# Performance work log

Measured on AMD Instinct MI355X. Metric: run time of the kernel, lower is better.

## Reference

```python
import jax, jax.numpy as jnp
import numpy as np

EMBED_DIM = 1024
NUM_HEADS = 16
HEAD_DIM = EMBED_DIM // NUM_HEADS  # 64
NUM_FEATURES = 32
POLY_DIM = 16
NUM_QUAD = 2
EPS = 1e-06
C = 2.0 + EPS
B = 4096


def setup_inputs() -> dict:
    key = jax.random.key(0)
    kx, k1, k2 = jax.random.split(key, 3)
    x = jax.random.normal(kx, (B, EMBED_DIM), dtype=jnp.float32)
    omega = jax.random.normal(k1, (NUM_QUAD, NUM_HEADS, HEAD_DIM, NUM_FEATURES), dtype=jnp.float32)
    omega = omega / jnp.sqrt(float(HEAD_DIM))
    anchors = jax.random.normal(k2, (POLY_DIM, HEAD_DIM), dtype=jnp.float32)
    anchors = anchors / jnp.linalg.norm(anchors, axis=-1, keepdims=True)
    nodes, weights = np.polynomial.laguerre.laggauss(NUM_QUAD)
    nodes = np.maximum(nodes, 0.01)
    weights = np.maximum(weights, 0.01)
    quad_nodes = jnp.array(nodes, dtype=jnp.float32) / C
    quad_weights = jnp.array(weights, dtype=jnp.float32) / C
    return {"x": x, "omega": omega, "anchors": anchors,
            "quad_nodes": quad_nodes, "quad_weights": quad_weights}


def reference(x, omega, anchors, quad_nodes, quad_weights):
    Bsz = x.shape[0]
    # [B, H, D], safe-normalize over head_dim
    xr = x.reshape(Bsz, NUM_HEADS, HEAD_DIM)
    norm = jnp.linalg.norm(xr, axis=-1, keepdims=True)
    xn = xr / jnp.maximum(norm, 1e-4)
    # polynomial features: [B, H, P]
    poly_proj = jnp.clip(jnp.einsum('bhd,pd->bhp', xn, anchors), -1.0, 1.0)
    poly_feat = poly_proj ** 2 / jnp.sqrt(float(POLY_DIM))
    # positive random features: [R, B, H, M]
    prf_proj = jnp.einsum('bhd,rhdm->rbhm', xn, omega)
    s = jnp.maximum(quad_nodes.reshape(-1, 1, 1, 1), 1e-06)
    exp_arg = jnp.clip(prf_proj * jnp.sqrt(2.0 * s) - s, -20.0, 20.0)
    prf_feat = jnp.exp(exp_arg) / jnp.sqrt(NUM_FEATURES + 1e-06)
    prf_feat = prf_feat * jnp.sqrt(jnp.maximum(quad_weights.reshape(-1, 1, 1, 1), 1e-06))
    # fused outer product over quadrature nodes: [R, B, H, P, M]
    fused = poly_feat[None, :, :, :, None] * prf_feat[:, :, :, None, :]
    # concat over r along last axis == r-major flatten: [B, R*H*P*M]
    return jnp.transpose(fused, (1, 0, 2, 3, 4)).reshape(Bsz, -1)
```

## Files before the change

### kernel.cpp

```cpp
#include <hip/hip_runtime.h>

#define NHEADS 16
#define HDIM   64
#define NFEAT  32
#define PDIM   16
#define NQUAD  2
#define GB     8
#define WAVES_PB 4

typedef float f32x4 __attribute__((ext_vector_type(4)));

__global__ __launch_bounds__(256, 3)
void slay_kernel(const float* __restrict__ x,
                 const float* __restrict__ omega,
                 const float* __restrict__ anchors,
                 const float* __restrict__ qn,
                 const float* __restrict__ qw,
                 float* __restrict__ out)
{
    __shared__ __align__(16) float s_xn [WAVES_PB][64];
    __shared__ __align__(16) float s_prf[WAVES_PB][64];
    __shared__ __align__(16) float s_poly[WAVES_PB][16];

    const int tid  = threadIdx.x;
    const int wv   = tid >> 6;
    const int lane = tid & 63;
    const int h    = blockIdx.x & 15;
    const int b0   = ((blockIdx.x >> 4) * WAVES_PB + wv) * GB;

    const int r = lane >> 5;
    const int m = lane & 31;
    const int p = lane & 15;
    const int g = lane >> 4;

    const float sR     = fmaxf(qn[r], 1e-6f);
    const float sq2s   = sqrtf(2.0f * sR);
    const float scaleR = sqrtf(fmaxf(qw[r], 1e-6f)) / sqrtf(32.0f + 1e-6f);

    float om[64];
    {
        const float* oc = omega + ((size_t)(r * NHEADS + h) * HDIM) * NFEAT + m;
        #pragma unroll
        for (int d = 0; d < 64; ++d) om[d] = oc[(size_t)d * NFEAT];
    }
    float an[16];
    {
        const float* ac = anchors + p * HDIM + g * 16;
        #pragma unroll
        for (int dd = 0; dd < 16; ++dd) an[dd] = ac[dd];
    }

    float xvv[GB];
    {
        const float* xb = x + (size_t)b0 * (NHEADS * HDIM) + h * HDIM + lane;
        #pragma unroll
        for (int bb = 0; bb < GB; ++bb) xvv[bb] = xb[(size_t)bb * (NHEADS * HDIM)];
    }

    #pragma unroll
    for (int bb = 0; bb < GB; ++bb) {
        const int b = b0 + bb;

        float ss = xvv[bb] * xvv[bb];
        #pragma unroll
        for (int off = 32; off > 0; off >>= 1) ss += __shfl_xor(ss, off, 64);
        const float xn = xvv[bb] / fmaxf(sqrtf(ss), 1e-4f);

        __builtin_amdgcn_wave_barrier();
        s_xn[wv][lane] = xn;
        __builtin_amdgcn_wave_barrier();

        float a0 = 0.f, a1 = 0.f, a2 = 0.f, a3 = 0.f;
        #pragma unroll
        for (int d = 0; d < 64; d += 4) {
            const float s0 = __uint_as_float(__builtin_amdgcn_readlane(__float_as_uint(xn), d + 0));
            const float s1 = __uint_as_float(__builtin_amdgcn_readlane(__float_as_uint(xn), d + 1));
            const float s2 = __uint_as_float(__builtin_amdgcn_readlane(__float_as_uint(xn), d + 2));
            const float s3 = __uint_as_float(__builtin_amdgcn_readlane(__float_as_uint(xn), d + 3));
            a0 = fmaf(s0, om[d + 0], a0);
            a1 = fmaf(s1, om[d + 1], a1);
            a2 = fmaf(s2, om[d + 2], a2);
            a3 = fmaf(s3, om[d + 3], a3);
        }
        const float accR = (a0 + a1) + (a2 + a3);

        float p0 = 0.f, p1 = 0.f, p2 = 0.f, p3 = 0.f;
        #pragma unroll
        for (int q4 = 0; q4 < 4; ++q4) {
            const f32x4 xq = *(const f32x4*)&s_xn[wv][g * 16 + q4 * 4];
            p0 = fmaf(xq.x, an[q4 * 4 + 0], p0);
            p1 = fmaf(xq.y, an[q4 * 4 + 1], p1);
            p2 = fmaf(xq.z, an[q4 * 4 + 2], p2);
            p3 = fmaf(xq.w, an[q4 * 4 + 3], p3);
        }
        float accP = (p0 + p1) + (p2 + p3);
        accP += __shfl_xor(accP, 16, 64);
        accP += __shfl_xor(accP, 32, 64);

        const float arg  = fminf(fmaxf(accR * sq2s - sR, -20.f), 20.f);
        const float prf  = expf(arg) * scaleR;
        const float pc   = fminf(fmaxf(accP, -1.f), 1.f);
        const float poly = pc * pc * 0.25f;

        __builtin_amdgcn_wave_barrier();
        s_prf[wv][lane] = prf;
        if (lane < 16) s_poly[wv][lane] = poly;
        __builtin_amdgcn_wave_barrier();

        float* ob = out + (size_t)b * (NQUAD * NHEADS * PDIM * NFEAT)
                        + (size_t)h * (PDIM * NFEAT);
        #pragma unroll
        for (int i4 = 0; i4 < 4; ++i4) {
            const int rr = i4 >> 1;
            const int pp = (i4 * 8 + (lane >> 3)) & 15;
            const float pf = s_poly[wv][pp];
            const f32x4 pr = *(const f32x4*)&s_prf[wv][rr * 32 + (lane & 7) * 4];
            f32x4 v;
            v.x = pf * pr.x; v.y = pf * pr.y; v.z = pf * pr.z; v.w = pf * pr.w;
            *(f32x4*)(ob + (size_t)rr * (NHEADS * PDIM * NFEAT)
                         + (i4 & 1) * 256 + lane * 4) = v;
        }
    }
}

extern "C" void kernel_launch(void* const* d_in, const int* in_sizes, int n_in,
                              void* d_out, int out_size, void* d_ws, size_t ws_size,
                              hipStream_t stream)
{
    const float* x       = (const float*)d_in[0];
    const float* omega   = (const float*)d_in[1];
    const float* anchors = (const float*)d_in[2];
    const float* qn      = (const float*)d_in[3];
    const float* qw      = (const float*)d_in[4];
    float* out = (float*)d_out;

    const int Bsz = in_sizes[0] / (NHEADS * HDIM);
    dim3 grid((Bsz / (WAVES_PB * GB)) * NHEADS);
    slay_kernel<<<grid, 256, 0, stream>>>(x, omega, anchors, qn, qw, out);
}
```

Measured before the change: 62.65 us.

## Split into feature kernel plus coalesced expand kernel via workspace

Computes prf and poly features in a first kernel and stores them in a workspace buffer. A second elementwise kernel then writes the outer-product output with fully linear, coalesced f32x4 stores. The goal is to separate the compute-heavy feature stage from the write-bandwidth-bound expansion so each can run at its own occupancy. The cost is extra workspace traffic and a second launch, and the old fused kernel is kept as a fallback when the workspace is too small.

Measured after the change: 76.15 us. 21.5% more time.

```diff
diff --git a/kernel.cpp b/kernel.cpp
--- a/kernel.cpp
+++ b/kernel.cpp
@@ -11,16 +11,15 @@
 typedef float f32x4 __attribute__((ext_vector_type(4)));
 
 __global__ __launch_bounds__(256, 3)
-void slay_kernel(const float* __restrict__ x,
-                 const float* __restrict__ omega,
-                 const float* __restrict__ anchors,
-                 const float* __restrict__ qn,
-                 const float* __restrict__ qw,
-                 float* __restrict__ out)
-{
-    __shared__ __align__(16) float s_xn [WAVES_PB][64];
-    __shared__ __align__(16) float s_prf[WAVES_PB][64];
-    __shared__ __align__(16) float s_poly[WAVES_PB][16];
+void slay_features(const float* __restrict__ x,
+                   const float* __restrict__ omega,
+                   const float* __restrict__ anchors,
+                   const float* __restrict__ qn,
+                   const float* __restrict__ qw,
+                   float* __restrict__ prf_ws,
+                   float* __restrict__ poly_ws)
+{
+    __shared__ __align__(16) float s_xn[WAVES_PB][64];
 
     const int tid  = threadIdx.x;
     const int wv   = tid >> 6;
@@ -102,6 +101,128 @@
         const float pc   = fminf(fmaxf(accP, -1.f), 1.f);
         const float poly = pc * pc * 0.25f;
 
+        prf_ws[(size_t)b * 1024 + r * 512 + h * 32 + m] = prf;
+        if (lane < 16)
+            poly_ws[(size_t)b * 256 + h * 16 + p] = poly;
+    }
+}
+
+__global__ __launch_bounds__(256)
+void slay_expand(const float* __restrict__ prf_ws,
+                 const float* __restrict__ poly_ws,
+                 float* __restrict__ out)
+{
+    const f32x4* __restrict__ prf4 = (const f32x4*)prf_ws;
+    f32x4* __restrict__ out4 = (f32x4*)out;
+
+    const int j0 = blockIdx.x * 1024 + threadIdx.x;
+    #pragma unroll
+    for (int k = 0; k < 4; ++k) {
+        const int j = j0 + k * 256;
+        const int b  = j >> 12;
+        const int q  = j & 4095;
+        const int rr = q >> 11;
+        const int hh = (q >> 7) & 15;
+        const int pp = (q >> 3) & 15;
+        const int mg = q & 7;
+        const float pf = poly_ws[(b << 8) | (hh << 4) | pp];
+        const f32x4 pr = prf4[(b << 8) | (rr << 7) | (hh << 3) | mg];
+        f32x4 v;
+        v.x = pf * pr.x; v.y = pf * pr.y; v.z = pf * pr.z; v.w = pf * pr.w;
+        out4[j] = v;
+    }
+}
+
+__global__ __launch_bounds__(256, 3)
+void slay_fused(const float* __restrict__ x,
+                const float* __restrict__ omega,
+                const float* __restrict__ anchors,
+                const float* __restrict__ qn,
+                const float* __restrict__ qw,
+                float* __restrict__ out)
+{
+    __shared__ __align__(16) float s_xn [WAVES_PB][64];
+    __shared__ __align__(16) float s_prf[WAVES_PB][64];
+    __shared__ __align__(16) float s_poly[WAVES_PB][16];
+
+    const int tid  = threadIdx.x;
+    const int wv   = tid >> 6;
+    const int lane = tid & 63;
+    const int h    = blockIdx.x & 15;
+    const int b0   = ((blockIdx.x >> 4) * WAVES_PB + wv) * GB;
+
+    const int r = lane >> 5;
+    const int m = lane & 31;
+    const int p = lane & 15;
+    const int g = lane >> 4;
+
+    const float sR     = fmaxf(qn[r], 1e-6f);
+    const float sq2s   = sqrtf(2.0f * sR);
+    const float scaleR = sqrtf(fmaxf(qw[r], 1e-6f)) / sqrtf(32.0f + 1e-6f);
+
+    float om[64];
+    {
+        const float* oc = omega + ((size_t)(r * NHEADS + h) * HDIM) * NFEAT + m;
+        #pragma unroll
+        for (int d = 0; d < 64; ++d) om[d] = oc[(size_t)d * NFEAT];
+    }
+    float an[16];
+    {
+        const float* ac = anchors + p * HDIM + g * 16;
+        #pragma unroll
+        for (int dd = 0; dd < 16; ++dd) an[dd] = ac[dd];
+    }
+    float xvv[GB];
+    {
+        const float* xb = x + (size_t)b0 * (NHEADS * HDIM) + h * HDIM + lane;
+        #pragma unroll
+        for (int bb = 0; bb < GB; ++bb) xvv[bb] = xb[(size_t)bb * (NHEADS * HDIM)];
+    }
+
+    #pragma unroll
+    for (int bb = 0; bb < GB; ++bb) {
+        const int b = b0 + bb;
+        float ss = xvv[bb] * xvv[bb];
+        #pragma unroll
+        for (int off = 32; off > 0; off >>= 1) ss += __shfl_xor(ss, off, 64);
+        const float xn = xvv[bb] / fmaxf(sqrtf(ss), 1e-4f);
+
+        __builtin_amdgcn_wave_barrier();
+        s_xn[wv][lane] = xn;
+        __builtin_amdgcn_wave_barrier();
+
+        float a0 = 0.f, a1 = 0.f, a2 = 0.f, a3 = 0.f;
+        #pragma unroll
+        for (int d = 0; d < 64; d += 4) {
+            const float s0 = __uint_as_float(__builtin_amdgcn_readlane(__float_as_uint(xn), d + 0));
+            const float s1 = __uint_as_float(__builtin_amdgcn_readlane(__float_as_uint(xn), d + 1));
+            const float s2 = __uint_as_float(__builtin_amdgcn_readlane(__float_as_uint(xn), d + 2));
+            const float s3 = __uint_as_float(__builtin_amdgcn_readlane(__float_as_uint(xn), d + 3));
+            a0 = fmaf(s0, om[d + 0], a0);
+            a1 = fmaf(s1, om[d + 1], a1);
+            a2 = fmaf(s2, om[d + 2], a2);
+            a3 = fmaf(s3, om[d + 3], a3);
+        }
+        const float accR = (a0 + a1) + (a2 + a3);
+
+        float p0 = 0.f, p1 = 0.f, p2 = 0.f, p3 = 0.f;
+        #pragma unroll
+        for (int q4 = 0; q4 < 4; ++q4) {
+            const f32x4 xq = *(const f32x4*)&s_xn[wv][g * 16 + q4 * 4];
+            p0 = fmaf(xq.x, an[q4 * 4 + 0], p0);
+            p1 = fmaf(xq.y, an[q4 * 4 + 1], p1);
+            p2 = fmaf(xq.z, an[q4 * 4 + 2], p2);
+            p3 = fmaf(xq.w, an[q4 * 4 + 3], p3);
+        }
+        float accP = (p0 + p1) + (p2 + p3);
+        accP += __shfl_xor(accP, 16, 64);
+        accP += __shfl_xor(accP, 32, 64);
+
+        const float arg  = fminf(fmaxf(accR * sq2s - sR, -20.f), 20.f);
+        const float prf  = expf(arg) * scaleR;
+        const float pc   = fminf(fmaxf(accP, -1.f), 1.f);
+        const float poly = pc * pc * 0.25f;
+
         __builtin_amdgcn_wave_barrier();
         s_prf[wv][lane] = prf;
         if (lane < 16) s_poly[wv][lane] = poly;
@@ -135,6 +256,21 @@
     float* out = (float*)d_out;
 
     const int Bsz = in_sizes[0] / (NHEADS * HDIM);
-    dim3 grid((Bsz / (WAVES_PB * GB)) * NHEADS);
-    slay_kernel<<<grid, 256, 0, stream>>>(x, omega, anchors, qn, qw, out);
-}
+    const size_t prf_elems  = (size_t)Bsz * NQUAD * NHEADS * NFEAT;
+    const size_t poly_elems = (size_t)Bsz * NHEADS * PDIM;
+    const size_t need = (prf_elems + poly_elems) * sizeof(float);
+
+    if (ws_size >= need) {
+        float* prf_ws  = (float*)d_ws;
+        float* poly_ws = prf_ws + prf_elems;
+        dim3 gridA((Bsz / (WAVES_PB * GB)) * NHEADS);
+        slay_features<<<gridA, 256, 0, stream>>>(x, omega, anchors, qn, qw,
+                                                 prf_ws, poly_ws);
+        const int total_f32x4 = out_size / 4;
+        dim3 gridB(total_f32x4 / 1024);
+        slay_expand<<<gridB, 256, 0, stream>>>(prf_ws, poly_ws, out);
+    } else {
+        dim3 grid((Bsz / (WAVES_PB * GB)) * NHEADS);
+        slay_fused<<<grid, 256, 0, stream>>>(x, omega, anchors, qn, qw, out);
+    }
+}
```
